# Kernel tuning notes

Measured on AMD Instinct MI355X. Metric: run time of the kernel, lower is better.

The kernel has to match this reference:

```python
import jax, jax.numpy as jnp
import numpy as np

DIM = 128
BATCH = 1048576
EPS = 1e-08


def setup_inputs() -> dict:
    key = jax.random.key(0)
    k1, k2 = jax.random.split(key)
    x = jax.random.normal(k1, (BATCH, DIM), dtype=jnp.float32)
    v_vectors = jax.random.normal(k2, (DIM, DIM), dtype=jnp.float32)
    scale = jnp.ones((1,), dtype=jnp.float32)
    diag_scale = jnp.ones((DIM,), dtype=jnp.float32)
    return {"x": x, "v_vectors": v_vectors, "scale": scale, "diag_scale": diag_scale}


def _build_Q(v_vectors, eps=EPS):
    # Q = H(v_0) @ H(v_1) @ ... @ H(v_{dim-1}), v_i = columns of v_vectors.
    # Q @ (I - 2 v v^T) = Q - 2 (Q v) v^T  -> avoid forming each H explicitly,
    # identical math to the original loop.
    dim = v_vectors.shape[0]
    vs = v_vectors.T  # rows of vs == columns of v_vectors, scan order preserved

    def step(Q, v):
        v = v / (jnp.linalg.norm(v) + eps)
        Qv = Q @ v
        return Q - 2.0 * jnp.outer(Qv, v), None

    Q0 = jnp.eye(dim, dtype=v_vectors.dtype)
    Q, _ = jax.lax.scan(step, Q0, vs)
    return Q


def reference(x, v_vectors, scale, diag_scale):
    Q = _build_Q(v_vectors)
    s = scale[0]
    # W = (Q @ diag(diag_scale)) * s  == Q scaled column-wise
    W = Q * (diag_scale * s)
    y = x @ W  # [B, dim]
    logdet = jnp.sum(jnp.log(jnp.abs(diag_scale * s) + EPS))
    return y, logdet
```

## Files before the change

### kernel.cpp

```cpp
#include <hip/hip_runtime.h>
#include <math.h>

#define DIM 128
#define BATCH 1048576
#define WT_STRIDE 136
#define VT_STRIDE 132
#define GEMM_GRID 512
#define NTILES (BATCH / 128)
#define TILES_PER_BLOCK (NTILES / GEMM_GRID)

typedef float f32x4 __attribute__((ext_vector_type(4)));
typedef short bf16x8 __attribute__((ext_vector_type(8)));

__device__ __forceinline__ unsigned short f2bf(float f) {
    unsigned u = __builtin_bit_cast(unsigned, f);
    u += 0x7FFFu + ((u >> 16) & 1u);
    return (unsigned short)(u >> 16);
}

__global__ __launch_bounds__(256, 1) void build_w_kernel(
    const float* __restrict__ vvec,
    const float* __restrict__ scale_p,
    const float* __restrict__ diag,
    unsigned short* __restrict__ wt,
    float* __restrict__ logdet_out)
{
    __shared__ float vt[DIM * VT_STRIDE];

    const int t    = threadIdx.x;
    const int r    = t >> 1;
    const int c0   = (t & 1) * 64;
    const int lane = t & 63;

    for (int idx = t; idx < DIM * DIM; idx += 256) {
        int j = idx >> 7;
        int i = idx & 127;
        vt[i * VT_STRIDE + j] = vvec[idx];
    }

    float q[64];
    #pragma unroll
    for (int j = 0; j < 64; ++j) q[j] = (c0 + j == r) ? 1.0f : 0.0f;

    __syncthreads();

    for (int i = 0; i < DIM; ++i) {
        const float* __restrict__ v = &vt[i * VT_STRIDE];

        float na = v[lane], nb = v[lane + 64];
        float ss = na * na + nb * nb;
        #pragma unroll
        for (int m = 32; m >= 1; m >>= 1) ss += __shfl_xor(ss, m, 64);
        const float sc = 1.0f / (sqrtf(ss) + 1e-8f);

        float vv[64];
        #pragma unroll
        for (int k = 0; k < 16; ++k) {
            f32x4 w = *(const f32x4*)(v + c0 + 4 * k);
            vv[4*k]   = w[0]; vv[4*k+1] = w[1];
            vv[4*k+2] = w[2]; vv[4*k+3] = w[3];
        }

        float d0 = 0.f, d1 = 0.f, d2 = 0.f, d3 = 0.f;
        #pragma unroll
        for (int k = 0; k < 16; ++k) {
            d0 += q[4*k]   * vv[4*k];
            d1 += q[4*k+1] * vv[4*k+1];
            d2 += q[4*k+2] * vv[4*k+2];
            d3 += q[4*k+3] * vv[4*k+3];
        }
        float dot = (d0 + d1) + (d2 + d3);
        dot += __shfl_xor(dot, 1, 64);

        const float coef = 2.0f * sc * sc * dot;
        #pragma unroll
        for (int j = 0; j < 64; ++j) q[j] -= coef * vv[j];
    }

    const float s = scale_p[0];
    #pragma unroll
    for (int j = 0; j < 64; ++j) {
        const int c = c0 + j;
        wt[c * WT_STRIDE + r] = f2bf(q[j] * diag[c] * s);
    }

    if (t < 64) {
        float ld = logf(fabsf(diag[t] * s) + 1e-8f)
                 + logf(fabsf(diag[t + 64] * s) + 1e-8f);
        #pragma unroll
        for (int m = 32; m >= 1; m >>= 1) ld += __shfl_xor(ld, m, 64);
        if (t == 0) *logdet_out = ld;
    }
}

__global__ __launch_bounds__(256, 2) void gemm_kernel(
    const float* __restrict__ x,
    const unsigned short* __restrict__ wt,
    float* __restrict__ y)
{
    __shared__ unsigned short wlds[DIM * WT_STRIDE];

    const int t = threadIdx.x;

    const int total4 = DIM * WT_STRIDE / 8;
    for (int idx = t; idx < total4; idx += 256) {
        ((f32x4*)wlds)[idx] = ((const f32x4*)wt)[idx];
    }

    const int wave = t >> 6;
    const int lane = t & 63;
    const int n15  = lane & 15;
    const int quad = lane >> 4;

    auto loadx = [&](f32x4 (&xb)[2][8], int tileIdx) {
        const long rowbase = (long)tileIdx * 128 + wave * 32;
        #pragma unroll
        for (int rt = 0; rt < 2; ++rt) {
            const float* xrow = x + (rowbase + rt * 16 + n15) * DIM + quad * 8;
            #pragma unroll
            for (int kc = 0; kc < 4; ++kc) {
                xb[rt][kc * 2]     = *(const f32x4*)(xrow + kc * 32);
                xb[rt][kc * 2 + 1] = *(const f32x4*)(xrow + kc * 32 + 4);
            }
        }
    };

    auto compute_store = [&](const f32x4 (&xb)[2][8], int tileIdx) {
        const long rowbase = (long)tileIdx * 128 + wave * 32;

        f32x4 acc[2][8];
        #pragma unroll
        for (int rt = 0; rt < 2; ++rt)
            #pragma unroll
            for (int ct = 0; ct < 8; ++ct)
                acc[rt][ct] = (f32x4)0.0f;

        #pragma unroll
        for (int kc = 0; kc < 4; ++kc) {
            bf16x8 afrag[2];
            #pragma unroll
            for (int rt = 0; rt < 2; ++rt) {
                const f32x4 lo = xb[rt][kc * 2];
                const f32x4 hi = xb[rt][kc * 2 + 1];
                bf16x8 f;
                f[0] = (short)f2bf(lo[0]); f[1] = (short)f2bf(lo[1]);
                f[2] = (short)f2bf(lo[2]); f[3] = (short)f2bf(lo[3]);
                f[4] = (short)f2bf(hi[0]); f[5] = (short)f2bf(hi[1]);
                f[6] = (short)f2bf(hi[2]); f[7] = (short)f2bf(hi[3]);
                afrag[rt] = f;
            }
            const int koff = kc * 32 + quad * 8;
            #pragma unroll
            for (int ct = 0; ct < 8; ++ct) {
                const bf16x8 bfrag = *(const bf16x8*)&wlds[(ct * 16 + n15) * WT_STRIDE + koff];
                acc[0][ct] = __builtin_amdgcn_mfma_f32_16x16x32_bf16(afrag[0], bfrag, acc[0][ct], 0, 0, 0);
                acc[1][ct] = __builtin_amdgcn_mfma_f32_16x16x32_bf16(afrag[1], bfrag, acc[1][ct], 0, 0, 0);
            }
        }

        #pragma unroll
        for (int rt = 0; rt < 2; ++rt) {
            #pragma unroll
            for (int reg = 0; reg < 4; ++reg) {
                float* yrow = y + (rowbase + rt * 16 + quad * 4 + reg) * DIM;
                #pragma unroll
                for (int ct = 0; ct < 8; ++ct) {
                    yrow[ct * 16 + n15] = acc[rt][ct][reg];
                }
            }
        }
    };

    f32x4 xa[2][8], xb[2][8];

    loadx(xa, blockIdx.x);
    __syncthreads();

    for (int kk = 0; kk < TILES_PER_BLOCK / 2; ++kk) {
        const int t0 = blockIdx.x + (2 * kk)     * GEMM_GRID;
        const int t1 = blockIdx.x + (2 * kk + 1) * GEMM_GRID;
        loadx(xb, t1);
        compute_store(xa, t0);
        if (kk + 1 < TILES_PER_BLOCK / 2)
            loadx(xa, blockIdx.x + (2 * kk + 2) * GEMM_GRID);
        compute_store(xb, t1);
    }
}

extern "C" void kernel_launch(void* const* d_in, const int* in_sizes, int n_in,
                              void* d_out, int out_size, void* d_ws, size_t ws_size,
                              hipStream_t stream) {
    const float* x     = (const float*)d_in[0];
    const float* vvec  = (const float*)d_in[1];
    const float* scale = (const float*)d_in[2];
    const float* diag  = (const float*)d_in[3];

    float* y = (float*)d_out;
    float* logdet = y + (size_t)BATCH * DIM;
    unsigned short* wt = (unsigned short*)d_ws;

    build_w_kernel<<<1, 256, 0, stream>>>(vvec, scale, diag, wt, logdet);
    gemm_kernel<<<GEMM_GRID, 256, 0, stream>>>(x, wt, y);
}
```

Baseline: 964.4 us.

## Shrink GEMM tiles to 64 rows, raise occupancy, precompute norms, nontemporal stores

The GEMM kernel now handles 64-row tiles with one 16-row strip per wave, doubles the grid to 1024 blocks and declares 4 blocks per CU. This cuts per-thread registers so more waves can hide memory latency. Output stores become nontemporal, and the first x tile is loaded before the W copy into LDS. The build kernel precomputes all Householder vector norms up front instead of a shuffle reduction per step, and splits the dot product into 8 partial sums; each wave now reuses every B fragment read from LDS for only one MFMA, so LDS traffic per flop doubles.

```diff
diff --git a/kernel.cpp b/kernel.cpp
--- a/kernel.cpp
+++ b/kernel.cpp
@@ -5,8 +5,9 @@
 #define BATCH 1048576
 #define WT_STRIDE 136
 #define VT_STRIDE 132
-#define GEMM_GRID 512
-#define NTILES (BATCH / 128)
+#define GEMM_GRID 1024
+#define ROWS_PER_TILE 64
+#define NTILES (BATCH / ROWS_PER_TILE)
 #define TILES_PER_BLOCK (NTILES / GEMM_GRID)
 
 typedef float f32x4 __attribute__((ext_vector_type(4)));
@@ -26,11 +27,11 @@
     float* __restrict__ logdet_out)
 {
     __shared__ float vt[DIM * VT_STRIDE];
-
-    const int t    = threadIdx.x;
-    const int r    = t >> 1;
-    const int c0   = (t & 1) * 64;
-    const int lane = t & 63;
+    __shared__ float sc_lds[DIM];
+
+    const int t  = threadIdx.x;
+    const int r  = t >> 1;
+    const int c0 = (t & 1) * 64;
 
     for (int idx = t; idx < DIM * DIM; idx += 256) {
         int j = idx >> 7;
@@ -44,14 +45,21 @@
 
     __syncthreads();
 
+    if (t < DIM) {
+        const float* v = &vt[t * VT_STRIDE];
+        float s0 = 0.f, s1 = 0.f, s2 = 0.f, s3 = 0.f;
+        #pragma unroll
+        for (int k = 0; k < 32; ++k) {
+            f32x4 w = *(const f32x4*)(v + 4 * k);
+            s0 += w[0] * w[0]; s1 += w[1] * w[1];
+            s2 += w[2] * w[2]; s3 += w[3] * w[3];
+        }
+        sc_lds[t] = 1.0f / (sqrtf((s0 + s1) + (s2 + s3)) + 1e-8f);
+    }
+    __syncthreads();
+
     for (int i = 0; i < DIM; ++i) {
         const float* __restrict__ v = &vt[i * VT_STRIDE];
-
-        float na = v[lane], nb = v[lane + 64];
-        float ss = na * na + nb * nb;
-        #pragma unroll
-        for (int m = 32; m >= 1; m >>= 1) ss += __shfl_xor(ss, m, 64);
-        const float sc = 1.0f / (sqrtf(ss) + 1e-8f);
 
         float vv[64];
         #pragma unroll
@@ -61,17 +69,22 @@
             vv[4*k+2] = w[2]; vv[4*k+3] = w[3];
         }
 
-        float d0 = 0.f, d1 = 0.f, d2 = 0.f, d3 = 0.f;
-        #pragma unroll
-        for (int k = 0; k < 16; ++k) {
-            d0 += q[4*k]   * vv[4*k];
-            d1 += q[4*k+1] * vv[4*k+1];
-            d2 += q[4*k+2] * vv[4*k+2];
-            d3 += q[4*k+3] * vv[4*k+3];
-        }
-        float dot = (d0 + d1) + (d2 + d3);
+        float d0=0.f,d1=0.f,d2=0.f,d3=0.f,d4=0.f,d5=0.f,d6=0.f,d7=0.f;
+        #pragma unroll
+        for (int k = 0; k < 8; ++k) {
+            d0 += q[8*k]   * vv[8*k];
+            d1 += q[8*k+1] * vv[8*k+1];
+            d2 += q[8*k+2] * vv[8*k+2];
+            d3 += q[8*k+3] * vv[8*k+3];
+            d4 += q[8*k+4] * vv[8*k+4];
+            d5 += q[8*k+5] * vv[8*k+5];
+            d6 += q[8*k+6] * vv[8*k+6];
+            d7 += q[8*k+7] * vv[8*k+7];
+        }
+        float dot = ((d0+d1)+(d2+d3)) + ((d4+d5)+(d6+d7));
         dot += __shfl_xor(dot, 1, 64);
 
+        const float sc   = sc_lds[i];
         const float coef = 2.0f * sc * sc * dot;
         #pragma unroll
         for (int j = 0; j < 64; ++j) q[j] -= coef * vv[j];
@@ -93,91 +106,74 @@
     }
 }
 
-__global__ __launch_bounds__(256, 2) void gemm_kernel(
+__global__ __launch_bounds__(256, 4) void gemm_kernel(
     const float* __restrict__ x,
     const unsigned short* __restrict__ wt,
     float* __restrict__ y)
 {
     __shared__ unsigned short wlds[DIM * WT_STRIDE];
 
-    const int t = threadIdx.x;
-
-    const int total4 = DIM * WT_STRIDE / 8;
-    for (int idx = t; idx < total4; idx += 256) {
-        ((f32x4*)wlds)[idx] = ((const f32x4*)wt)[idx];
-    }
-
+    const int t    = threadIdx.x;
     const int wave = t >> 6;
     const int lane = t & 63;
     const int n15  = lane & 15;
     const int quad = lane >> 4;
 
-    auto loadx = [&](f32x4 (&xb)[2][8], int tileIdx) {
-        const long rowbase = (long)tileIdx * 128 + wave * 32;
-        #pragma unroll
-        for (int rt = 0; rt < 2; ++rt) {
-            const float* xrow = x + (rowbase + rt * 16 + n15) * DIM + quad * 8;
-            #pragma unroll
-            for (int kc = 0; kc < 4; ++kc) {
-                xb[rt][kc * 2]     = *(const f32x4*)(xrow + kc * 32);
-                xb[rt][kc * 2 + 1] = *(const f32x4*)(xrow + kc * 32 + 4);
-            }
+    auto loadx = [&](f32x4 (&xb)[8], int tileIdx) {
+        const long row = (long)tileIdx * ROWS_PER_TILE + wave * 16 + n15;
+        const float* xrow = x + row * DIM + quad * 8;
+        #pragma unroll
+        for (int kc = 0; kc < 4; ++kc) {
+            xb[kc * 2]     = *(const f32x4*)(xrow + kc * 32);
+            xb[kc * 2 + 1] = *(const f32x4*)(xrow + kc * 32 + 4);
         }
     };
 
-    auto compute_store = [&](const f32x4 (&xb)[2][8], int tileIdx) {
-        const long rowbase = (long)tileIdx * 128 + wave * 32;
-
-        f32x4 acc[2][8];
-        #pragma unroll
-        for (int rt = 0; rt < 2; ++rt)
-            #pragma unroll
-            for (int ct = 0; ct < 8; ++ct)
-                acc[rt][ct] = (f32x4)0.0f;
+    auto compute_store = [&](const f32x4 (&xb)[8], int tileIdx) {
+        f32x4 acc[8];
+        #pragma unroll
+        for (int ct = 0; ct < 8; ++ct) acc[ct] = (f32x4)0.0f;
 
         #pragma unroll
         for (int kc = 0; kc < 4; ++kc) {
-            bf16x8 afrag[2];
-            #pragma unroll
-            for (int rt = 0; rt < 2; ++rt) {
-                const f32x4 lo = xb[rt][kc * 2];
-                const f32x4 hi = xb[rt][kc * 2 + 1];
-                bf16x8 f;
-                f[0] = (short)f2bf(lo[0]); f[1] = (short)f2bf(lo[1]);
-                f[2] = (short)f2bf(lo[2]); f[3] = (short)f2bf(lo[3]);
-                f[4] = (short)f2bf(hi[0]); f[5] = (short)f2bf(hi[1]);
-                f[6] = (short)f2bf(hi[2]); f[7] = (short)f2bf(hi[3]);
-                afrag[rt] = f;
-            }
+            const f32x4 lo = xb[kc * 2];
+            const f32x4 hi = xb[kc * 2 + 1];
+            bf16x8 f;
+            f[0] = (short)f2bf(lo[0]); f[1] = (short)f2bf(lo[1]);
+            f[2] = (short)f2bf(lo[2]); f[3] = (short)f2bf(lo[3]);
+            f[4] = (short)f2bf(hi[0]); f[5] = (short)f2bf(hi[1]);
+            f[6] = (short)f2bf(hi[2]); f[7] = (short)f2bf(hi[3]);
             const int koff = kc * 32 + quad * 8;
             #pragma unroll
             for (int ct = 0; ct < 8; ++ct) {
                 const bf16x8 bfrag = *(const bf16x8*)&wlds[(ct * 16 + n15) * WT_STRIDE + koff];
-                acc[0][ct] = __builtin_amdgcn_mfma_f32_16x16x32_bf16(afrag[0], bfrag, acc[0][ct], 0, 0, 0);
-                acc[1][ct] = __builtin_amdgcn_mfma_f32_16x16x32_bf16(afrag[1], bfrag, acc[1][ct], 0, 0, 0);
+                acc[ct] = __builtin_amdgcn_mfma_f32_16x16x32_bf16(f, bfrag, acc[ct], 0, 0, 0);
             }
         }
 
-        #pragma unroll
-        for (int rt = 0; rt < 2; ++rt) {
+        const long rowbase = (long)tileIdx * ROWS_PER_TILE + wave * 16;
+        #pragma unroll
+        for (int reg = 0; reg < 4; ++reg) {
+            float* yrow = y + (rowbase + quad * 4 + reg) * DIM;
             #pragma unroll
-            for (int reg = 0; reg < 4; ++reg) {
-                float* yrow = y + (rowbase + rt * 16 + quad * 4 + reg) * DIM;
-                #pragma unroll
-                for (int ct = 0; ct < 8; ++ct) {
-                    yrow[ct * 16 + n15] = acc[rt][ct][reg];
-                }
+            for (int ct = 0; ct < 8; ++ct) {
+                __builtin_nontemporal_store(acc[ct][reg], &yrow[ct * 16 + n15]);
             }
         }
     };
 
-    f32x4 xa[2][8], xb[2][8];
+    f32x4 xa[8], xb[8];
 
     loadx(xa, blockIdx.x);
+    const int total4 = DIM * WT_STRIDE / 8;
+    for (int idx = t; idx < total4; idx += 256) {
+        ((f32x4*)wlds)[idx] = ((const f32x4*)wt)[idx];
+    }
     __syncthreads();
 
+    #pragma unroll 1
     for (int kk = 0; kk < TILES_PER_BLOCK / 2; ++kk) {
-        const int t0 = blockIdx.x + (2 * kk)     * GEMM_GRID;
+        const int t0 = blockIdx.x + (2 * kk) * GEMM_GRID;
         const int t1 = blockIdx.x + (2 * kk + 1) * GEMM_GRID;
         loadx(xb, t1);
         compute_store(xa, t0);
```

Result: slower. 1.177 ms (+22.0%).
